# Kernel optimization log

Hardware: AMD Instinct MI355X
Metric: run time of the kernel (lower is better)

The kernel has to match this reference:

```python
import jax, jax.numpy as jnp
import numpy as np

K = 3
NUM_STEP_COMBO = 5
BN_EPS = 1e-5


def setup_inputs() -> dict:
    key = jax.random.key(0)
    ks = jax.random.split(key, 10)
    N, E, D, H, O, G = 100000, 1600000, 48, 128, 12, 64
    x = jax.random.normal(ks[0], (N, D), dtype=jnp.float32)
    edge_index = jax.random.randint(ks[1], (2, E), 0, N, dtype=jnp.int64)
    batch = jnp.sort(jax.random.randint(ks[2], (N,), 0, G, dtype=jnp.int64))
    # ChebConv params: one [D, D] weight per Chebyshev order, shared bias
    W = jax.random.normal(ks[3], (K, D, D), dtype=jnp.float32) * 0.1
    b = jnp.zeros((D,), dtype=jnp.float32)
    gamma = jnp.ones((D,), dtype=jnp.float32)
    beta = jnp.zeros((D,), dtype=jnp.float32)
    W1 = jax.random.normal(ks[4], (D, H), dtype=jnp.float32) * 0.1
    b1 = jnp.zeros((H,), dtype=jnp.float32)
    W2 = jax.random.normal(ks[5], (H, O), dtype=jnp.float32) * 0.1
    b2 = jnp.zeros((O,), dtype=jnp.float32)
    return {"x": x, "edge_index": edge_index, "batch": batch, "num_graphs": 64,
            "W": W, "b": b, "gamma": gamma, "beta": beta,
            "W1": W1, "b1": b1, "W2": W2, "b2": b2}


def cheb_conv(x, row, col, W, b):
    # PyG ChebConv, sym norm, lambda_max=2 => L_hat = -D^{-1/2} A D^{-1/2}
    N = x.shape[0]
    deg = jax.ops.segment_sum(jnp.ones_like(row, dtype=x.dtype), row, num_segments=N)
    dinv = jnp.where(deg > 0, jax.lax.rsqrt(jnp.maximum(deg, 1.0)), 0.0)
    norm = (-dinv[row] * dinv[col])[:, None]  # [E,1] edge weights of L_hat

    def lhat(v):  # sparse matvec: gather neighbors, scale, scatter-add
        return jax.ops.segment_sum(norm * v[col], row, num_segments=N)

    Tx0 = x
    Tx1 = lhat(x)
    out = Tx0 @ W[0] + Tx1 @ W[1]
    Txkm2, Txkm1 = Tx0, Tx1
    for k in range(2, W.shape[0]):
        Txk = 2.0 * lhat(Txkm1) - Txkm2
        out = out + Txk @ W[k]
        Txkm2, Txkm1 = Txkm1, Txk
    return out + b


def reference(x, edge_index, batch, num_graphs, W, b, gamma, beta, W1, b1, W2, b2):
    row, col = edge_index[0], edge_index[1]
    N = x.shape[0]
    out = x
    for _ in range(NUM_STEP_COMBO):
        t = jax.nn.relu(cheb_conv(out, row, col, W, b))
        # BatchNorm1d (training-mode stats over all nodes, biased var)
        mean = jnp.mean(t, axis=0)
        var = jnp.mean((t - mean) ** 2, axis=0)
        t = gamma * (t - mean) * jax.lax.rsqrt(var + BN_EPS) + beta
        # graph_max_pool: per-node max over incoming neighbor features
        m = jax.ops.segment_max(t[col], row, num_segments=N)
        out = jnp.where(jnp.isneginf(m), 0.0, m)  # empty segments -> 0
    g = jax.ops.segment_sum(out, batch, num_segments=num_graphs)  # global_add_pool
    h = jax.nn.relu(g @ W1 + b1)
    return h @ W2 + b2
```

## Files before the change

kernel.cpp:

```cpp
#include <hip/hip_runtime.h>
#include <hip/hip_bf16.h>

#define D 48
#define GNUM 64
#define HDIM 128
#define ODIM 12
#define BN_EPS 1e-5f

typedef _Float16 half2v __attribute__((ext_vector_type(2)));
typedef _Float16 half4v __attribute__((ext_vector_type(4)));
typedef _Float16 half8v __attribute__((ext_vector_type(8)));

#if __has_builtin(__builtin_amdgcn_fdot2)
#define FDOT2(a, b, c) __builtin_amdgcn_fdot2((a), (b), (c), false)
#else
#define FDOT2(a, b, c) ((c) + (float)(a)[0] * (float)(b)[0] + (float)(a)[1] * (float)(b)[1])
#endif


__global__ __launch_bounds__(256) void k_deg(const int* __restrict__ row, int* __restrict__ deg, int E) {
    int e = blockIdx.x * 256 + threadIdx.x;
    if (e < E) atomicAdd(&deg[row[e]], 1);
}

__global__ __launch_bounds__(256) void k_dinv(const int* __restrict__ deg, float* __restrict__ dinv, int N) {
    int i = blockIdx.x * 256 + threadIdx.x;
    if (i < N) dinv[i] = deg[i] > 0 ? rsqrtf((float)deg[i]) : 0.f;
}

__global__ __launch_bounds__(256) void k_scan1(const int* __restrict__ deg, int* __restrict__ incl,
                                               int* __restrict__ bsum, int N) {
    __shared__ int s[256];
    int i = blockIdx.x * 256 + threadIdx.x;
    s[threadIdx.x] = (i < N) ? deg[i] : 0;
    __syncthreads();
    for (int off = 1; off < 256; off <<= 1) {
        int t = (threadIdx.x >= off) ? s[threadIdx.x - off] : 0;
        __syncthreads();
        s[threadIdx.x] += t;
        __syncthreads();
    }
    if (i < N) incl[i] = s[threadIdx.x];
    if (threadIdx.x == 255) bsum[blockIdx.x] = s[255];
}

__global__ __launch_bounds__(512) void k_scan2(int* __restrict__ bsum, int nb) {
    __shared__ int s[512];
    int t = threadIdx.x;
    s[t] = (t < nb) ? bsum[t] : 0;
    __syncthreads();
    for (int off = 1; off < 512; off <<= 1) {
        int v = (t >= off) ? s[t - off] : 0;
        __syncthreads();
        s[t] += v;
        __syncthreads();
    }
    if (t < nb) bsum[t] = s[t];
}

__global__ __launch_bounds__(256) void k_scan3(const int* __restrict__ incl, const int* __restrict__ bsum,
                                               int* __restrict__ rowptr, int N) {
    int i = blockIdx.x * 256 + threadIdx.x;
    if (i < N) {
        int add = (blockIdx.x > 0) ? bsum[blockIdx.x - 1] : 0;
        rowptr[i + 1] = incl[i] + add;
    }
    if (i == 0) rowptr[0] = 0;
}

__global__ __launch_bounds__(256) void k_fill(const int* __restrict__ row, const int* __restrict__ col,
                                              const int* __restrict__ rowptr, int* __restrict__ fillc,
                                              const float* __restrict__ dinv, int2* __restrict__ epair, int E) {
    int e = blockIdx.x * 256 + threadIdx.x;
    if (e < E) {
        int r = row[e], c = col[e];
        int p = rowptr[r] + atomicAdd(&fillc[r], 1);
        epair[p] = make_int2(c, __float_as_int(dinv[c]));
    }
}

__global__ __launch_bounds__(256) void k_cvt(const float* __restrict__ x, _Float16* __restrict__ xh, int n4) {
    int i = blockIdx.x * 256 + threadIdx.x;
    if (i < n4) {
        float4 v = ((const float4*)x)[i];
        half4v h;
        h.x = (_Float16)v.x; h.y = (_Float16)v.y; h.z = (_Float16)v.z; h.w = (_Float16)v.w;
        ((half4v*)xh)[i] = h;
    }
}


__global__ __launch_bounds__(256) void k_lhat(const _Float16* __restrict__ cur, const int* __restrict__ rowptr,
                                              const int2* __restrict__ epair, const float* __restrict__ dinv,
                                              _Float16* __restrict__ tx1, int N) {
    int lane = threadIdx.x & 63;
    int i = (blockIdx.x * 256 + threadIdx.x) >> 6;
    if (i >= N) return;
    int q = lane & 15, slot = lane >> 4;
    int qc = q < 12 ? q : 11;
    int s = rowptr[i], e = rowptr[i + 1];
    float a0 = 0.f, a1 = 0.f, a2 = 0.f, a3 = 0.f;
    int p = s + slot;
    for (; p + 4 < e; p += 8) {
        int2 ea = epair[p];
        int2 eb = epair[p + 4];
        float wa = __int_as_float(ea.y), wb = __int_as_float(eb.y);
        half4v ha = *(const half4v*)(cur + (size_t)ea.x * D + qc * 4);
        half4v hb = *(const half4v*)(cur + (size_t)eb.x * D + qc * 4);
        a0 += wa * (float)ha.x + wb * (float)hb.x;
        a1 += wa * (float)ha.y + wb * (float)hb.y;
        a2 += wa * (float)ha.z + wb * (float)hb.z;
        a3 += wa * (float)ha.w + wb * (float)hb.w;
    }
    if (p < e) {
        int2 ea = epair[p];
        float wa = __int_as_float(ea.y);
        half4v ha = *(const half4v*)(cur + (size_t)ea.x * D + qc * 4);
        a0 += wa * (float)ha.x; a1 += wa * (float)ha.y; a2 += wa * (float)ha.z; a3 += wa * (float)ha.w;
    }
    a0 += __shfl_xor(a0, 16); a1 += __shfl_xor(a1, 16); a2 += __shfl_xor(a2, 16); a3 += __shfl_xor(a3, 16);
    a0 += __shfl_xor(a0, 32); a1 += __shfl_xor(a1, 32); a2 += __shfl_xor(a2, 32); a3 += __shfl_xor(a3, 32);
    if (lane < 12) {
        float sc = -dinv[i];
        half4v o;
        o.x = (_Float16)(sc * a0); o.y = (_Float16)(sc * a1);
        o.z = (_Float16)(sc * a2); o.w = (_Float16)(sc * a3);
        *(half4v*)(tx1 + (size_t)i * D + lane * 4) = o;
    }
}

__global__ __launch_bounds__(256) void k_gather2(const _Float16* __restrict__ tx0, const _Float16* __restrict__ tx1,
                                                 const int* __restrict__ rowptr, const int2* __restrict__ epair,
                                                 const float* __restrict__ dinv, _Float16* __restrict__ tx2, int N) {
    int lane = threadIdx.x & 63;
    int i = (blockIdx.x * 256 + threadIdx.x) >> 6;
    if (i >= N) return;
    int q = lane & 15, slot = lane >> 4;
    int qc = q < 12 ? q : 11;
    int s = rowptr[i], e = rowptr[i + 1];
    float a0 = 0.f, a1 = 0.f, a2 = 0.f, a3 = 0.f;
    int p = s + slot;
    for (; p + 4 < e; p += 8) {
        int2 ea = epair[p];
        int2 eb = epair[p + 4];
        float wa = __int_as_float(ea.y), wb = __int_as_float(eb.y);
        half4v ha = *(const half4v*)(tx1 + (size_t)ea.x * D + qc * 4);
        half4v hb = *(const half4v*)(tx1 + (size_t)eb.x * D + qc * 4);
        a0 += wa * (float)ha.x + wb * (float)hb.x;
        a1 += wa * (float)ha.y + wb * (float)hb.y;
        a2 += wa * (float)ha.z + wb * (float)hb.z;
        a3 += wa * (float)ha.w + wb * (float)hb.w;
    }
    if (p < e) {
        int2 ea = epair[p];
        float wa = __int_as_float(ea.y);
        half4v ha = *(const half4v*)(tx1 + (size_t)ea.x * D + qc * 4);
        a0 += wa * (float)ha.x; a1 += wa * (float)ha.y; a2 += wa * (float)ha.z; a3 += wa * (float)ha.w;
    }
    a0 += __shfl_xor(a0, 16); a1 += __shfl_xor(a1, 16); a2 += __shfl_xor(a2, 16); a3 += __shfl_xor(a3, 16);
    a0 += __shfl_xor(a0, 32); a1 += __shfl_xor(a1, 32); a2 += __shfl_xor(a2, 32); a3 += __shfl_xor(a3, 32);
    if (lane < 12) {
        float sc = -2.f * dinv[i];
        half4v h0 = *(const half4v*)(tx0 + (size_t)i * D + lane * 4);
        half4v o;
        o.x = (_Float16)(sc * a0 - (float)h0.x); o.y = (_Float16)(sc * a1 - (float)h0.y);
        o.z = (_Float16)(sc * a2 - (float)h0.z); o.w = (_Float16)(sc * a3 - (float)h0.w);
        *(half4v*)(tx2 + (size_t)i * D + lane * 4) = o;
    }
}


__global__ __launch_bounds__(256) void k_dense(const _Float16* __restrict__ tx0, const _Float16* __restrict__ tx1,
                                               const _Float16* __restrict__ tx2, const float* __restrict__ W,
                                               const float* __restrict__ b, _Float16* __restrict__ tbuf, int N) {
    __shared__ half2v WH2[72 * D];
    __shared__ float bL[D];
    for (int t = threadIdx.x; t < 72 * D; t += 256) {
        int kp = t / D, j = t % D;
        half2v w;
        w.x = (_Float16)W[(2 * kp) * D + j];
        w.y = (_Float16)W[(2 * kp + 1) * D + j];
        WH2[t] = w;
    }
    if (threadIdx.x < D) bL[threadIdx.x] = b[threadIdx.x];
    __syncthreads();

    int base = (blockIdx.x * 256 + threadIdx.x) * 2;
    if (base >= N) return;
    bool two = (base + 1) < N;

    const _Float16* rowsA[3] = {tx0 + (size_t)base * D, tx1 + (size_t)base * D, tx2 + (size_t)base * D};
    size_t off2 = two ? D : 0;

    float acc0[D], acc1[D];
#pragma unroll
    for (int j = 0; j < D; ++j) { acc0[j] = bL[j]; acc1[j] = bL[j]; }

    for (int s = 0; s < 3; ++s) {
        const half2v* xa = (const half2v*)rowsA[s];
        const half2v* xb = (const half2v*)(rowsA[s] + off2);
#pragma unroll 4
        for (int g = 0; g < 24; ++g) {
            half2v va = xa[g], vb = xb[g];
            int kp = s * 24 + g;
            const half8v* wr = (const half8v*)&WH2[kp * D];
#pragma unroll
            for (int jc = 0; jc < 12; ++jc) {
                half8v w = wr[jc];
                half2v w0; w0.x = w[0]; w0.y = w[1];
                half2v w1; w1.x = w[2]; w1.y = w[3];
                half2v w2; w2.x = w[4]; w2.y = w[5];
                half2v w3; w3.x = w[6]; w3.y = w[7];
                acc0[jc * 4 + 0] = FDOT2(va, w0, acc0[jc * 4 + 0]);
                acc0[jc * 4 + 1] = FDOT2(va, w1, acc0[jc * 4 + 1]);
                acc0[jc * 4 + 2] = FDOT2(va, w2, acc0[jc * 4 + 2]);
                acc0[jc * 4 + 3] = FDOT2(va, w3, acc0[jc * 4 + 3]);
                acc1[jc * 4 + 0] = FDOT2(vb, w0, acc1[jc * 4 + 0]);
                acc1[jc * 4 + 1] = FDOT2(vb, w1, acc1[jc * 4 + 1]);
                acc1[jc * 4 + 2] = FDOT2(vb, w2, acc1[jc * 4 + 2]);
                acc1[jc * 4 + 3] = FDOT2(vb, w3, acc1[jc * 4 + 3]);
            }
        }
    }

    _Float16* o0 = tbuf + (size_t)base * D;
#pragma unroll
    for (int jc = 0; jc < 12; ++jc) {
        half4v h;
        h.x = (_Float16)fmaxf(acc0[jc * 4 + 0], 0.f);
        h.y = (_Float16)fmaxf(acc0[jc * 4 + 1], 0.f);
        h.z = (_Float16)fmaxf(acc0[jc * 4 + 2], 0.f);
        h.w = (_Float16)fmaxf(acc0[jc * 4 + 3], 0.f);
        *(half4v*)(o0 + jc * 4) = h;
    }
    if (two) {
        _Float16* o1 = o0 + D;
#pragma unroll
        for (int jc = 0; jc < 12; ++jc) {
            half4v h;
            h.x = (_Float16)fmaxf(acc1[jc * 4 + 0], 0.f);
            h.y = (_Float16)fmaxf(acc1[jc * 4 + 1], 0.f);
            h.z = (_Float16)fmaxf(acc1[jc * 4 + 2], 0.f);
            h.w = (_Float16)fmaxf(acc1[jc * 4 + 3], 0.f);
            *(half4v*)(o1 + jc * 4) = h;
        }
    }
}


__global__ __launch_bounds__(256) void k_bnstat(const _Float16* __restrict__ tbuf, float* __restrict__ bnstats, int N) {
    __shared__ float red[2 * D];
    if (threadIdx.x < 2 * D) red[threadIdx.x] = 0.f;
    __syncthreads();
    int tid = blockIdx.x * 256 + threadIdx.x;
    int q = tid % 12;
    int n0 = tid / 12;
    int stride = (gridDim.x * 256) / 12;
    float s0 = 0, s1 = 0, s2 = 0, s3 = 0, q0 = 0, q1 = 0, q2 = 0, q3 = 0;
    for (int n = n0; n < N; n += stride) {
        half4v h = *(const half4v*)(tbuf + (size_t)n * D + q * 4);
        float f0 = (float)h.x, f1 = (float)h.y, f2 = (float)h.z, f3 = (float)h.w;
        s0 += f0; s1 += f1; s2 += f2; s3 += f3;
        q0 += f0 * f0; q1 += f1 * f1; q2 += f2 * f2; q3 += f3 * f3;
    }
    atomicAdd(&red[q * 4 + 0], s0); atomicAdd(&red[q * 4 + 1], s1);
    atomicAdd(&red[q * 4 + 2], s2); atomicAdd(&red[q * 4 + 3], s3);
    atomicAdd(&red[D + q * 4 + 0], q0); atomicAdd(&red[D + q * 4 + 1], q1);
    atomicAdd(&red[D + q * 4 + 2], q2); atomicAdd(&red[D + q * 4 + 3], q3);
    __syncthreads();
    if (threadIdx.x < 2 * D) atomicAdd(&bnstats[threadIdx.x], red[threadIdx.x]);
}

__global__ __launch_bounds__(64) void k_bnfin(float* __restrict__ bnstats, const float* __restrict__ gamma,
                                              const float* __restrict__ beta, float* __restrict__ ss, float Ninv) {
    int t = threadIdx.x;
    if (t < D) {
        float mean = bnstats[t] * Ninv;
        float var = bnstats[D + t] * Ninv - mean * mean;
        var = fmaxf(var, 0.f);
        float sc = gamma[t] * rsqrtf(var + BN_EPS);
        ss[t] = sc;
        ss[D + t] = beta[t] - mean * sc;
        bnstats[t] = 0.f;
        bnstats[D + t] = 0.f;
    }
}


__global__ __launch_bounds__(256) void k_pool(const _Float16* __restrict__ tbuf, const int* __restrict__ rowptr,
                                              const int2* __restrict__ epair, const float* __restrict__ ss,
                                              _Float16* __restrict__ outh, int N) {
    int lane = threadIdx.x & 63;
    int i = (blockIdx.x * 256 + threadIdx.x) >> 6;
    if (i >= N) return;
    int q = lane & 15, slot = lane >> 4;
    int qc = q < 12 ? q : 11;
    int s = rowptr[i], e = rowptr[i + 1];
    float m0 = -3.4e38f, m1 = -3.4e38f, m2 = -3.4e38f, m3 = -3.4e38f;
    float n0 = 3.4e38f, n1 = 3.4e38f, n2 = 3.4e38f, n3 = 3.4e38f;
    int p = s + slot;
    for (; p + 4 < e; p += 8) {
        int ca = epair[p].x, cb = epair[p + 4].x;
        half4v ha = *(const half4v*)(tbuf + (size_t)ca * D + qc * 4);
        half4v hb = *(const half4v*)(tbuf + (size_t)cb * D + qc * 4);
        float a0 = (float)ha.x, a1 = (float)ha.y, a2 = (float)ha.z, a3 = (float)ha.w;
        float b0 = (float)hb.x, b1 = (float)hb.y, b2 = (float)hb.z, b3 = (float)hb.w;
        m0 = fmaxf(m0, fmaxf(a0, b0)); m1 = fmaxf(m1, fmaxf(a1, b1));
        m2 = fmaxf(m2, fmaxf(a2, b2)); m3 = fmaxf(m3, fmaxf(a3, b3));
        n0 = fminf(n0, fminf(a0, b0)); n1 = fminf(n1, fminf(a1, b1));
        n2 = fminf(n2, fminf(a2, b2)); n3 = fminf(n3, fminf(a3, b3));
    }
    if (p < e) {
        int ca = epair[p].x;
        half4v ha = *(const half4v*)(tbuf + (size_t)ca * D + qc * 4);
        float a0 = (float)ha.x, a1 = (float)ha.y, a2 = (float)ha.z, a3 = (float)ha.w;
        m0 = fmaxf(m0, a0); m1 = fmaxf(m1, a1); m2 = fmaxf(m2, a2); m3 = fmaxf(m3, a3);
        n0 = fminf(n0, a0); n1 = fminf(n1, a1); n2 = fminf(n2, a2); n3 = fminf(n3, a3);
    }
    m0 = fmaxf(m0, __shfl_xor(m0, 16)); m1 = fmaxf(m1, __shfl_xor(m1, 16));
    m2 = fmaxf(m2, __shfl_xor(m2, 16)); m3 = fmaxf(m3, __shfl_xor(m3, 16));
    m0 = fmaxf(m0, __shfl_xor(m0, 32)); m1 = fmaxf(m1, __shfl_xor(m1, 32));
    m2 = fmaxf(m2, __shfl_xor(m2, 32)); m3 = fmaxf(m3, __shfl_xor(m3, 32));
    n0 = fminf(n0, __shfl_xor(n0, 16)); n1 = fminf(n1, __shfl_xor(n1, 16));
    n2 = fminf(n2, __shfl_xor(n2, 16)); n3 = fminf(n3, __shfl_xor(n3, 16));
    n0 = fminf(n0, __shfl_xor(n0, 32)); n1 = fminf(n1, __shfl_xor(n1, 32));
    n2 = fminf(n2, __shfl_xor(n2, 32)); n3 = fminf(n3, __shfl_xor(n3, 32));
    if (lane < 12) {
        float4 sc = *(const float4*)(ss + lane * 4);
        float4 sh = *(const float4*)(ss + D + lane * 4);
        half4v o;
        if (s == e) {
            o.x = (_Float16)0.f; o.y = (_Float16)0.f; o.z = (_Float16)0.f; o.w = (_Float16)0.f;
        } else {
            float v0 = (sc.x >= 0.f) ? sc.x * m0 + sh.x : sc.x * n0 + sh.x;
            float v1 = (sc.y >= 0.f) ? sc.y * m1 + sh.y : sc.y * n1 + sh.y;
            float v2 = (sc.z >= 0.f) ? sc.z * m2 + sh.z : sc.z * n2 + sh.z;
            float v3 = (sc.w >= 0.f) ? sc.w * m3 + sh.w : sc.w * n3 + sh.w;
            o.x = (_Float16)v0; o.y = (_Float16)v1; o.z = (_Float16)v2; o.w = (_Float16)v3;
        }
        *(half4v*)(outh + (size_t)i * D + lane * 4) = o;
    }
}


__global__ __launch_bounds__(256) void k_gpool(const _Float16* __restrict__ outh, const int* __restrict__ batch,
                                               float* __restrict__ g, int N, int chunk) {
    int lane = threadIdx.x & 63;
    int wid = (blockIdx.x * 256 + threadIdx.x) >> 6;
    int start = wid * chunk;
    if (start >= N || lane >= 12) return;
    int end = start + chunk;
    if (end > N) end = N;
    int curb = batch[start];
    float a0 = 0.f, a1 = 0.f, a2 = 0.f, a3 = 0.f;
    for (int i = start; i < end; ++i) {
        int bi = batch[i];
        if (bi != curb) {
            atomicAdd(&g[curb * D + lane * 4 + 0], a0); atomicAdd(&g[curb * D + lane * 4 + 1], a1);
            atomicAdd(&g[curb * D + lane * 4 + 2], a2); atomicAdd(&g[curb * D + lane * 4 + 3], a3);
            curb = bi; a0 = a1 = a2 = a3 = 0.f;
        }
        half4v h = *(const half4v*)(outh + (size_t)i * D + lane * 4);
        a0 += (float)h.x; a1 += (float)h.y; a2 += (float)h.z; a3 += (float)h.w;
    }
    atomicAdd(&g[curb * D + lane * 4 + 0], a0); atomicAdd(&g[curb * D + lane * 4 + 1], a1);
    atomicAdd(&g[curb * D + lane * 4 + 2], a2); atomicAdd(&g[curb * D + lane * 4 + 3], a3);
}

__global__ __launch_bounds__(256) void k_mlp(const float* __restrict__ g, const float* __restrict__ W1,
                                             const float* __restrict__ b1, const float* __restrict__ W2,
                                             const float* __restrict__ b2, float* __restrict__ out) {
    __shared__ float gL[GNUM * D];
    __shared__ float hL[GNUM * HDIM];
    __shared__ float W1L[D * HDIM];
    int t = threadIdx.x;
    for (int i = t; i < GNUM * D; i += 256) gL[i] = g[i];
    for (int i = t; i < D * HDIM; i += 256) W1L[i] = W1[i];
    __syncthreads();
    for (int i = t; i < GNUM * HDIM; i += 256) {
        int gi = i >> 7, hj = i & 127;
        float a = b1[hj];
        for (int k = 0; k < D; ++k) a += gL[gi * D + k] * W1L[k * HDIM + hj];
        hL[i] = fmaxf(a, 0.f);
    }
    __syncthreads();
    for (int i = t; i < GNUM * ODIM; i += 256) {
        int gi = i / ODIM, oj = i % ODIM;
        float a = b2[oj];
        for (int k = 0; k < HDIM; ++k) a += hL[gi * HDIM + k] * W2[k * ODIM + oj];
        out[i] = a;
    }
}


extern "C" void kernel_launch(void* const* d_in, const int* in_sizes, int n_in,
                              void* d_out, int out_size, void* d_ws, size_t ws_size,
                              hipStream_t stream) {
    const float* x     = (const float*)d_in[0];
    const int*   ei    = (const int*)d_in[1];
    const int*   batch = (const int*)d_in[2];
    const float* W     = (const float*)d_in[4];
    const float* b     = (const float*)d_in[5];
    const float* gamma = (const float*)d_in[6];
    const float* beta  = (const float*)d_in[7];
    const float* W1    = (const float*)d_in[8];
    const float* b1    = (const float*)d_in[9];
    const float* W2    = (const float*)d_in[10];
    const float* b2    = (const float*)d_in[11];

    int N = in_sizes[0] / D;
    int E = in_sizes[1] / 2;
    const int* row = ei;
    const int* col = ei + E;

    char* w = (char*)d_ws;
    auto alloc = [&](size_t bytes) { char* p = w; w += (bytes + 255) & ~(size_t)255; return p; };
    int*       deg     = (int*)alloc((size_t)N * 4);
    float*     dinv    = (float*)alloc((size_t)N * 4);
    int*       fillc   = (int*)alloc((size_t)N * 4);
    int*       incl    = (int*)alloc((size_t)N * 4);
    int*       bsum    = (int*)alloc(4096);
    int*       rowptr  = (int*)alloc((size_t)(N + 1) * 4);
    int2*      epair   = (int2*)alloc((size_t)E * 8);
    _Float16*  xh      = (_Float16*)alloc((size_t)N * D * 2 + 64);
    _Float16*  tx1h    = (_Float16*)alloc((size_t)N * D * 2 + 64);
    _Float16*  tx2h    = (_Float16*)alloc((size_t)N * D * 2 + 64);
    _Float16*  tbufh   = (_Float16*)alloc((size_t)N * D * 2 + 64);
    _Float16*  outh    = (_Float16*)alloc((size_t)N * D * 2 + 64);
    float*     bnstats = (float*)alloc(2 * D * 4);
    float*     ss      = (float*)alloc(2 * D * 4);
    float*     g       = (float*)alloc((size_t)GNUM * D * 4);

    hipMemsetAsync(deg, 0, (size_t)N * 4, stream);
    hipMemsetAsync(fillc, 0, (size_t)N * 4, stream);
    hipMemsetAsync(bnstats, 0, 2 * D * 4, stream);
    hipMemsetAsync(g, 0, (size_t)GNUM * D * 4, stream);

    int nbE = (E + 255) / 256;
    int nbN = (N + 255) / 256;

    k_deg<<<nbE, 256, 0, stream>>>(row, deg, E);
    k_dinv<<<nbN, 256, 0, stream>>>(deg, dinv, N);
    k_scan1<<<nbN, 256, 0, stream>>>(deg, incl, bsum, N);
    k_scan2<<<1, 512, 0, stream>>>(bsum, nbN);
    k_scan3<<<nbN, 256, 0, stream>>>(incl, bsum, rowptr, N);
    k_fill<<<nbE, 256, 0, stream>>>(row, col, rowptr, fillc, dinv, epair, E);
    int n4 = N * D / 4;
    k_cvt<<<(n4 + 255) / 256, 256, 0, stream>>>(x, xh, n4);

    int nbWave = (N * 64 + 255) / 256;
    int nbDense = ((N + 1) / 2 + 255) / 256;
    const _Float16* cur = xh;
    for (int step = 0; step < 5; ++step) {
        k_lhat<<<nbWave, 256, 0, stream>>>(cur, rowptr, epair, dinv, tx1h, N);
        k_gather2<<<nbWave, 256, 0, stream>>>(cur, tx1h, rowptr, epair, dinv, tx2h, N);
        k_dense<<<nbDense, 256, 0, stream>>>(cur, tx1h, tx2h, W, b, tbufh, N);
        k_bnstat<<<120, 256, 0, stream>>>(tbufh, bnstats, N);
        k_bnfin<<<1, 64, 0, stream>>>(bnstats, gamma, beta, ss, 1.f / (float)N);
        k_pool<<<nbWave, 256, 0, stream>>>(tbufh, rowptr, epair, ss, outh, N);
        cur = outh;
    }

    int chunk = 32;
    int nwaves = (N + chunk - 1) / chunk;
    int nbG = (nwaves * 64 + 255) / 256;
    k_gpool<<<nbG, 256, 0, stream>>>(outh, batch, g, N, chunk);
    k_mlp<<<1, 256, 0, stream>>>(g, W1, b1, W2, b2, (float*)d_out);
}
```

Baseline: 1.269 ms.

## Pre-scale features by dinv to drop per-edge weights and widen gathers to 16B

Producers now also write a copy of each feature row pre-multiplied by the node's dinv. This lets the sparse Laplacian gathers use a plain sum over neighbours, so the edge list shrinks from (col, weight) int2 pairs to bare column indices. The gather, second-order and max-pool kernels also switch from 8-byte half4 loads with 16 edge slots per wave to 16-byte half8 loads with 8 slots, halving the number of gather instructions. The cost is extra writes of the scaled copies in the convert, lhat and pool kernels, plus somewhat different fp16 rounding from scaling before the sum.

```diff
diff --git a/kernel.cpp b/kernel.cpp
--- a/kernel.cpp
+++ b/kernel.cpp
@@ -70,102 +70,113 @@
 
 __global__ __launch_bounds__(256) void k_fill(const int* __restrict__ row, const int* __restrict__ col,
                                               const int* __restrict__ rowptr, int* __restrict__ fillc,
-                                              const float* __restrict__ dinv, int2* __restrict__ epair, int E) {
+                                              int* __restrict__ ecol, int E) {
     int e = blockIdx.x * 256 + threadIdx.x;
     if (e < E) {
         int r = row[e], c = col[e];
         int p = rowptr[r] + atomicAdd(&fillc[r], 1);
-        epair[p] = make_int2(c, __float_as_int(dinv[c]));
-    }
-}
-
-__global__ __launch_bounds__(256) void k_cvt(const float* __restrict__ x, _Float16* __restrict__ xh, int n4) {
+        ecol[p] = c;
+    }
+}
+
+__global__ __launch_bounds__(256) void k_cvt(const float* __restrict__ x, const float* __restrict__ dinv,
+                                             _Float16* __restrict__ xh, _Float16* __restrict__ xs, int n4) {
     int i = blockIdx.x * 256 + threadIdx.x;
     if (i < n4) {
+        int node = i / 12;
+        float dv = dinv[node];
         float4 v = ((const float4*)x)[i];
-        half4v h;
+        half4v h, hs;
         h.x = (_Float16)v.x; h.y = (_Float16)v.y; h.z = (_Float16)v.z; h.w = (_Float16)v.w;
+        hs.x = (_Float16)(dv * v.x); hs.y = (_Float16)(dv * v.y);
+        hs.z = (_Float16)(dv * v.z); hs.w = (_Float16)(dv * v.w);
         ((half4v*)xh)[i] = h;
-    }
-}
-
-
-__global__ __launch_bounds__(256) void k_lhat(const _Float16* __restrict__ cur, const int* __restrict__ rowptr,
-                                              const int2* __restrict__ epair, const float* __restrict__ dinv,
-                                              _Float16* __restrict__ tx1, int N) {
+        ((half4v*)xs)[i] = hs;
+    }
+}
+
+
+__global__ __launch_bounds__(256) void k_lhat(const _Float16* __restrict__ curs, const int* __restrict__ rowptr,
+                                              const int* __restrict__ ecol, const float* __restrict__ dinv,
+                                              _Float16* __restrict__ tx1, _Float16* __restrict__ tx1s, int N) {
     int lane = threadIdx.x & 63;
     int i = (blockIdx.x * 256 + threadIdx.x) >> 6;
     if (i >= N) return;
-    int q = lane & 15, slot = lane >> 4;
-    int qc = q < 12 ? q : 11;
+    int q = lane & 7, slot = lane >> 3;
+    int qc = q < 6 ? q : 5;
     int s = rowptr[i], e = rowptr[i + 1];
-    float a0 = 0.f, a1 = 0.f, a2 = 0.f, a3 = 0.f;
+    float a[8] = {0.f, 0.f, 0.f, 0.f, 0.f, 0.f, 0.f, 0.f};
     int p = s + slot;
-    for (; p + 4 < e; p += 8) {
-        int2 ea = epair[p];
-        int2 eb = epair[p + 4];
-        float wa = __int_as_float(ea.y), wb = __int_as_float(eb.y);
-        half4v ha = *(const half4v*)(cur + (size_t)ea.x * D + qc * 4);
-        half4v hb = *(const half4v*)(cur + (size_t)eb.x * D + qc * 4);
-        a0 += wa * (float)ha.x + wb * (float)hb.x;
-        a1 += wa * (float)ha.y + wb * (float)hb.y;
-        a2 += wa * (float)ha.z + wb * (float)hb.z;
-        a3 += wa * (float)ha.w + wb * (float)hb.w;
+    for (; p + 8 < e; p += 16) {
+        int ca = ecol[p], cb = ecol[p + 8];
+        half8v ha = *(const half8v*)(curs + (size_t)ca * D + qc * 8);
+        half8v hb = *(const half8v*)(curs + (size_t)cb * D + qc * 8);
+#pragma unroll
+        for (int j = 0; j < 8; ++j) a[j] += (float)ha[j] + (float)hb[j];
     }
     if (p < e) {
-        int2 ea = epair[p];
-        float wa = __int_as_float(ea.y);
-        half4v ha = *(const half4v*)(cur + (size_t)ea.x * D + qc * 4);
-        a0 += wa * (float)ha.x; a1 += wa * (float)ha.y; a2 += wa * (float)ha.z; a3 += wa * (float)ha.w;
-    }
-    a0 += __shfl_xor(a0, 16); a1 += __shfl_xor(a1, 16); a2 += __shfl_xor(a2, 16); a3 += __shfl_xor(a3, 16);
-    a0 += __shfl_xor(a0, 32); a1 += __shfl_xor(a1, 32); a2 += __shfl_xor(a2, 32); a3 += __shfl_xor(a3, 32);
-    if (lane < 12) {
-        float sc = -dinv[i];
-        half4v o;
-        o.x = (_Float16)(sc * a0); o.y = (_Float16)(sc * a1);
-        o.z = (_Float16)(sc * a2); o.w = (_Float16)(sc * a3);
-        *(half4v*)(tx1 + (size_t)i * D + lane * 4) = o;
-    }
-}
-
-__global__ __launch_bounds__(256) void k_gather2(const _Float16* __restrict__ tx0, const _Float16* __restrict__ tx1,
-                                                 const int* __restrict__ rowptr, const int2* __restrict__ epair,
+        int ca = ecol[p];
+        half8v ha = *(const half8v*)(curs + (size_t)ca * D + qc * 8);
+#pragma unroll
+        for (int j = 0; j < 8; ++j) a[j] += (float)ha[j];
+    }
+#pragma unroll
+    for (int j = 0; j < 8; ++j) {
+        a[j] += __shfl_xor(a[j], 8);
+        a[j] += __shfl_xor(a[j], 16);
+        a[j] += __shfl_xor(a[j], 32);
+    }
+    if (lane < 6) {
+        float di = dinv[i];
+        half8v o, os;
+#pragma unroll
+        for (int j = 0; j < 8; ++j) {
+            float t = -di * a[j];
+            o[j] = (_Float16)t;
+            os[j] = (_Float16)(di * t);
+        }
+        *(half8v*)(tx1 + (size_t)i * D + lane * 8) = o;
+        *(half8v*)(tx1s + (size_t)i * D + lane * 8) = os;
+    }
+}
+
+__global__ __launch_bounds__(256) void k_gather2(const _Float16* __restrict__ tx0, const _Float16* __restrict__ tx1s,
+                                                 const int* __restrict__ rowptr, const int* __restrict__ ecol,
                                                  const float* __restrict__ dinv, _Float16* __restrict__ tx2, int N) {
     int lane = threadIdx.x & 63;
     int i = (blockIdx.x * 256 + threadIdx.x) >> 6;
     if (i >= N) return;
-    int q = lane & 15, slot = lane >> 4;
-    int qc = q < 12 ? q : 11;
+    int q = lane & 7, slot = lane >> 3;
+    int qc = q < 6 ? q : 5;
     int s = rowptr[i], e = rowptr[i + 1];
-    float a0 = 0.f, a1 = 0.f, a2 = 0.f, a3 = 0.f;
+    float a[8] = {0.f, 0.f, 0.f, 0.f, 0.f, 0.f, 0.f, 0.f};
     int p = s + slot;
-    for (; p + 4 < e; p += 8) {
-        int2 ea = epair[p];
-        int2 eb = epair[p + 4];
-        float wa = __int_as_float(ea.y), wb = __int_as_float(eb.y);
-        half4v ha = *(const half4v*)(tx1 + (size_t)ea.x * D + qc * 4);
-        half4v hb = *(const half4v*)(tx1 + (size_t)eb.x * D + qc * 4);
-        a0 += wa * (float)ha.x + wb * (float)hb.x;
-        a1 += wa * (float)ha.y + wb * (float)hb.y;
-        a2 += wa * (float)ha.z + wb * (float)hb.z;
-        a3 += wa * (float)ha.w + wb * (float)hb.w;
+    for (; p + 8 < e; p += 16) {
+        int ca = ecol[p], cb = ecol[p + 8];
+        half8v ha = *(const half8v*)(tx1s + (size_t)ca * D + qc * 8);
+        half8v hb = *(const half8v*)(tx1s + (size_t)cb * D + qc * 8);
+#pragma unroll
+        for (int j = 0; j < 8; ++j) a[j] += (float)ha[j] + (float)hb[j];
     }
     if (p < e) {
-        int2 ea = epair[p];
-        float wa = __int_as_float(ea.y);
-        half4v ha = *(const half4v*)(tx1 + (size_t)ea.x * D + qc * 4);
-        a0 += wa * (float)ha.x; a1 += wa * (float)ha.y; a2 += wa * (float)ha.z; a3 += wa * (float)ha.w;
-    }
-    a0 += __shfl_xor(a0, 16); a1 += __shfl_xor(a1, 16); a2 += __shfl_xor(a2, 16); a3 += __shfl_xor(a3, 16);
-    a0 += __shfl_xor(a0, 32); a1 += __shfl_xor(a1, 32); a2 += __shfl_xor(a2, 32); a3 += __shfl_xor(a3, 32);
-    if (lane < 12) {
+        int ca = ecol[p];
+        half8v ha = *(const half8v*)(tx1s + (size_t)ca * D + qc * 8);
+#pragma unroll
+        for (int j = 0; j < 8; ++j) a[j] += (float)ha[j];
+    }
+#pragma unroll
+    for (int j = 0; j < 8; ++j) {
+        a[j] += __shfl_xor(a[j], 8);
+        a[j] += __shfl_xor(a[j], 16);
+        a[j] += __shfl_xor(a[j], 32);
+    }
+    if (lane < 6) {
         float sc = -2.f * dinv[i];
-        half4v h0 = *(const half4v*)(tx0 + (size_t)i * D + lane * 4);
-        half4v o;
-        o.x = (_Float16)(sc * a0 - (float)h0.x); o.y = (_Float16)(sc * a1 - (float)h0.y);
-        o.z = (_Float16)(sc * a2 - (float)h0.z); o.w = (_Float16)(sc * a3 - (float)h0.w);
-        *(half4v*)(tx2 + (size_t)i * D + lane * 4) = o;
+        half8v h0 = *(const half8v*)(tx0 + (size_t)i * D + lane * 8);
+        half8v o;
+#pragma unroll
+        for (int j = 0; j < 8; ++j) o[j] = (_Float16)(sc * a[j] - (float)h0[j]);
+        *(half8v*)(tx2 + (size_t)i * D + lane * 8) = o;
     }
 }
 
@@ -288,57 +299,67 @@
 
 
 __global__ __launch_bounds__(256) void k_pool(const _Float16* __restrict__ tbuf, const int* __restrict__ rowptr,
-                                              const int2* __restrict__ epair, const float* __restrict__ ss,
-                                              _Float16* __restrict__ outh, int N) {
+                                              const int* __restrict__ ecol, const float* __restrict__ ss,
+                                              const float* __restrict__ dinv, _Float16* __restrict__ outh,
+                                              _Float16* __restrict__ outs, int N) {
     int lane = threadIdx.x & 63;
     int i = (blockIdx.x * 256 + threadIdx.x) >> 6;
     if (i >= N) return;
-    int q = lane & 15, slot = lane >> 4;
-    int qc = q < 12 ? q : 11;
+    int q = lane & 7, slot = lane >> 3;
+    int qc = q < 6 ? q : 5;
     int s = rowptr[i], e = rowptr[i + 1];
-    float m0 = -3.4e38f, m1 = -3.4e38f, m2 = -3.4e38f, m3 = -3.4e38f;
-    float n0 = 3.4e38f, n1 = 3.4e38f, n2 = 3.4e38f, n3 = 3.4e38f;
+    float mx[8], mn[8];
+#pragma unroll
+    for (int j = 0; j < 8; ++j) { mx[j] = -3.4e38f; mn[j] = 3.4e38f; }
     int p = s + slot;
-    for (; p + 4 < e; p += 8) {
-        int ca = epair[p].x, cb = epair[p + 4].x;
-        half4v ha = *(const half4v*)(tbuf + (size_t)ca * D + qc * 4);
-        half4v hb = *(const half4v*)(tbuf + (size_t)cb * D + qc * 4);
-        float a0 = (float)ha.x, a1 = (float)ha.y, a2 = (float)ha.z, a3 = (float)ha.w;
-        float b0 = (float)hb.x, b1 = (float)hb.y, b2 = (float)hb.z, b3 = (float)hb.w;
-        m0 = fmaxf(m0, fmaxf(a0, b0)); m1 = fmaxf(m1, fmaxf(a1, b1));
-        m2 = fmaxf(m2, fmaxf(a2, b2)); m3 = fmaxf(m3, fmaxf(a3, b3));
-        n0 = fminf(n0, fminf(a0, b0)); n1 = fminf(n1, fminf(a1, b1));
-        n2 = fminf(n2, fminf(a2, b2)); n3 = fminf(n3, fminf(a3, b3));
+    for (; p + 8 < e; p += 16) {
+        int ca = ecol[p], cb = ecol[p + 8];
+        half8v ha = *(const half8v*)(tbuf + (size_t)ca * D + qc * 8);
+        half8v hb = *(const half8v*)(tbuf + (size_t)cb * D + qc * 8);
+#pragma unroll
+        for (int j = 0; j < 8; ++j) {
+            float fa = (float)ha[j], fb = (float)hb[j];
+            mx[j] = fmaxf(mx[j], fmaxf(fa, fb));
+            mn[j] = fminf(mn[j], fminf(fa, fb));
+        }
     }
     if (p < e) {
-        int ca = epair[p].x;
-        half4v ha = *(const half4v*)(tbuf + (size_t)ca * D + qc * 4);
-        float a0 = (float)ha.x, a1 = (float)ha.y, a2 = (float)ha.z, a3 = (float)ha.w;
-        m0 = fmaxf(m0, a0); m1 = fmaxf(m1, a1); m2 = fmaxf(m2, a2); m3 = fmaxf(m3, a3);
-        n0 = fminf(n0, a0); n1 = fminf(n1, a1); n2 = fminf(n2, a2); n3 = fminf(n3, a3);
-    }
-    m0 = fmaxf(m0, __shfl_xor(m0, 16)); m1 = fmaxf(m1, __shfl_xor(m1, 16));
-    m2 = fmaxf(m2, __shfl_xor(m2, 16)); m3 = fmaxf(m3, __shfl_xor(m3, 16));
-    m0 = fmaxf(m0, __shfl_xor(m0, 32)); m1 = fmaxf(m1, __shfl_xor(m1, 32));
-    m2 = fmaxf(m2, __shfl_xor(m2, 32)); m3 = fmaxf(m3, __shfl_xor(m3, 32));
-    n0 = fminf(n0, __shfl_xor(n0, 16)); n1 = fminf(n1, __shfl_xor(n1, 16));
-    n2 = fminf(n2, __shfl_xor(n2, 16)); n3 = fminf(n3, __shfl_xor(n3, 16));
-    n0 = fminf(n0, __shfl_xor(n0, 32)); n1 = fminf(n1, __shfl_xor(n1, 32));
-    n2 = fminf(n2, __shfl_xor(n2, 32)); n3 = fminf(n3, __shfl_xor(n3, 32));
-    if (lane < 12) {
-        float4 sc = *(const float4*)(ss + lane * 4);
-        float4 sh = *(const float4*)(ss + D + lane * 4);
-        half4v o;
+        int ca = ecol[p];
+        half8v ha = *(const half8v*)(tbuf + (size_t)ca * D + qc * 8);
+#pragma unroll
+        for (int j = 0; j < 8; ++j) {
+            float fa = (float)ha[j];
+            mx[j] = fmaxf(mx[j], fa);
+            mn[j] = fminf(mn[j], fa);
+        }
+    }
+#pragma unroll
+    for (int j = 0; j < 8; ++j) {
+        mx[j] = fmaxf(mx[j], __shfl_xor(mx[j], 8));
+        mx[j] = fmaxf(mx[j], __shfl_xor(mx[j], 16));
+        mx[j] = fmaxf(mx[j], __shfl_xor(mx[j], 32));
+        mn[j] = fminf(mn[j], __shfl_xor(mn[j], 8));
+        mn[j] = fminf(mn[j], __shfl_xor(mn[j], 16));
+        mn[j] = fminf(mn[j], __shfl_xor(mn[j], 32));
+    }
+    if (lane < 6) {
+        float di = dinv[i];
+        half8v o, os;
         if (s == e) {
-            o.x = (_Float16)0.f; o.y = (_Float16)0.f; o.z = (_Float16)0.f; o.w = (_Float16)0.f;
+#pragma unroll
+            for (int j = 0; j < 8; ++j) { o[j] = (_Float16)0.f; os[j] = (_Float16)0.f; }
         } else {
-            float v0 = (sc.x >= 0.f) ? sc.x * m0 + sh.x : sc.x * n0 + sh.x;
-            float v1 = (sc.y >= 0.f) ? sc.y * m1 + sh.y : sc.y * n1 + sh.y;
-            float v2 = (sc.z >= 0.f) ? sc.z * m2 + sh.z : sc.z * n2 + sh.z;
-            float v3 = (sc.w >= 0.f) ? sc.w * m3 + sh.w : sc.w * n3 + sh.w;
-            o.x = (_Float16)v0; o.y = (_Float16)v1; o.z = (_Float16)v2; o.w = (_Float16)v3;
-        }
-        *(half4v*)(outh + (size_t)i * D + lane * 4) = o;
+#pragma unroll
+            for (int j = 0; j < 8; ++j) {
+                float scj = ss[lane * 8 + j];
+                float shj = ss[D + lane * 8 + j];
+                float v = (scj >= 0.f) ? scj * mx[j] + shj : scj * mn[j] + shj;
+                o[j] = (_Float16)v;
+                os[j] = (_Float16)(di * v);
+            }
+        }
+        *(half8v*)(outh + (size_t)i * D + lane * 8) = o;
+        *(half8v*)(outs + (size_t)i * D + lane * 8) = os;
     }
 }
 
@@ -421,12 +442,15 @@
     int*       incl    = (int*)alloc((size_t)N * 4);
     int*       bsum    = (int*)alloc(4096);
     int*       rowptr  = (int*)alloc((size_t)(N + 1) * 4);
-    int2*      epair   = (int2*)alloc((size_t)E * 8);
+    int*       ecol    = (int*)alloc((size_t)E * 4);
     _Float16*  xh      = (_Float16*)alloc((size_t)N * D * 2 + 64);
+    _Float16*  xs      = (_Float16*)alloc((size_t)N * D * 2 + 64);
     _Float16*  tx1h    = (_Float16*)alloc((size_t)N * D * 2 + 64);
+    _Float16*  tx1s    = (_Float16*)alloc((size_t)N * D * 2 + 64);
     _Float16*  tx2h    = (_Float16*)alloc((size_t)N * D * 2 + 64);
     _Float16*  tbufh   = (_Float16*)alloc((size_t)N * D * 2 + 64);
     _Float16*  outh    = (_Float16*)alloc((size_t)N * D * 2 + 64);
+    _Float16*  outs    = (_Float16*)alloc((size_t)N * D * 2 + 64);
     float*     bnstats = (float*)alloc(2 * D * 4);
     float*     ss      = (float*)alloc(2 * D * 4);
     float*     g       = (float*)alloc((size_t)GNUM * D * 4);
@@ -444,21 +468,23 @@
     k_scan1<<<nbN, 256, 0, stream>>>(deg, incl, bsum, N);
     k_scan2<<<1, 512, 0, stream>>>(bsum, nbN);
     k_scan3<<<nbN, 256, 0, stream>>>(incl, bsum, rowptr, N);
-    k_fill<<<nbE, 256, 0, stream>>>(row, col, rowptr, fillc, dinv, epair, E);
+    k_fill<<<nbE, 256, 0, stream>>>(row, col, rowptr, fillc, ecol, E);
     int n4 = N * D / 4;
-    k_cvt<<<(n4 + 255) / 256, 256, 0, stream>>>(x, xh, n4);
+    k_cvt<<<(n4 + 255) / 256, 256, 0, stream>>>(x, dinv, xh, xs, n4);
 
     int nbWave = (N * 64 + 255) / 256;
     int nbDense = ((N + 1) / 2 + 255) / 256;
-    const _Float16* cur = xh;
+    const _Float16* curh = xh;
+    const _Float16* curs = xs;
     for (int step = 0; step < 5; ++step) {
-        k_lhat<<<nbWave, 256, 0, stream>>>(cur, rowptr, epair, dinv, tx1h, N);
-        k_gather2<<<nbWave, 256, 0, stream>>>(cur, tx1h, rowptr, epair, dinv, tx2h, N);
-        k_dense<<<nbDense, 256, 0, stream>>>(cur, tx1h, tx2h, W, b, tbufh, N);
+        k_lhat<<<nbWave, 256, 0, stream>>>(curs, rowptr, ecol, dinv, tx1h, tx1s, N);
+        k_gather2<<<nbWave, 256, 0, stream>>>(curh, tx1s, rowptr, ecol, dinv, tx2h, N);
+        k_dense<<<nbDense, 256, 0, stream>>>(curh, tx1h, tx2h, W, b, tbufh, N);
         k_bnstat<<<120, 256, 0, stream>>>(tbufh, bnstats, N);
         k_bnfin<<<1, 64, 0, stream>>>(bnstats, gamma, beta, ss, 1.f / (float)N);
-        k_pool<<<nbWave, 256, 0, stream>>>(tbufh, rowptr, epair, ss, outh, N);
-        cur = outh;
+        k_pool<<<nbWave, 256, 0, stream>>>(tbufh, rowptr, ecol, ss, dinv, outh, outs, N);
+        curh = outh;
+        curs = outs;
     }
 
     int chunk = 32;
```

New measurement: 1.296 ms. 1.02x slower.
